# Kernel optimization log

Hardware: AMD Instinct MI355X
Metric: run time of the kernel (lower is better)

## Reference

```python
import jax, jax.numpy as jnp
import numpy as np

EPS = 1e-5

def _gather_particles(x, idx):
    # x: [B, C, M], idx: [B, N] -> [B, C, N]
    return jax.vmap(lambda a, i: a[:, i])(x, idx)

def _group_norm_dense(x, gamma, beta):
    # groups == channels (default GroupNorm(num_groups=out_channels)) -> per-channel over spatial
    m = x.mean(axis=(2, 3, 4), keepdims=True)
    v = x.var(axis=(2, 3, 4), keepdims=True)
    return (x - m) * jax.lax.rsqrt(v + EPS) * gamma[None, :, None, None, None] + beta[None, :, None, None, None]

def _group_norm_particles(x, gamma, beta):
    # x: [B, C, N]; per-channel norm over particle dim
    m = x.mean(axis=2, keepdims=True)
    v = x.var(axis=2, keepdims=True)
    return (x - m) * jax.lax.rsqrt(v + EPS) * gamma[None, :, None] + beta[None, :, None]

def _apr_conv(x, w, neighbor_idx):
    # x: [B, Cin, N]; w: [Cout, Cin, K]; neighbor_idx: [B, N, K]
    K = w.shape[2]
    out = jnp.zeros((x.shape[0], w.shape[0], x.shape[2]), x.dtype)
    for k in range(K):  # small fixed stencil
        xg = _gather_particles(x, neighbor_idx[:, :, k])  # [B, Cin, N]
        out = out + jnp.einsum('bcn,oc->bon', xg, w[:, :, k])
    return out

def setup_inputs() -> dict:
    key = jax.random.key(0)
    ks = jax.random.split(key, 12)
    B, Cin, D = 2, 64, 40
    Nc, Nf, K = 100_000, 400_000, 7
    Ch = Cin // 2  # 32
    Cout = 32
    S = D * D * D
    return {
        'x1': jax.random.normal(ks[0], (B, Cin, D, D, D), jnp.float32),
        'x2': jax.random.normal(ks[1], (B, Ch, Nf), jnp.float32),
        'w_reduce': jax.random.normal(ks[2], (Ch, Cin), jnp.float32) * 0.1,
        'gnr_gamma': jnp.ones((Ch,), jnp.float32),
        'gnr_beta': jnp.zeros((Ch,), jnp.float32),
        'w1': jax.random.normal(ks[3], (Cout, Cin, K), jnp.float32) * 0.1,
        'g1': jnp.ones((Cout,), jnp.float32),
        'b1': jnp.zeros((Cout,), jnp.float32),
        'w2': jax.random.normal(ks[4], (Cout, Cout, K), jnp.float32) * 0.1,
        'g2': jnp.ones((Cout,), jnp.float32),
        'b2': jnp.zeros((Cout,), jnp.float32),
        'sample_idx': jax.random.randint(ks[5], (B, Nc), 0, S, jnp.int32),
        'upsample_idx': jax.random.randint(ks[6], (B, Nf), 0, Nc, jnp.int32),
        'neighbor_idx': jax.random.randint(ks[7], (B, Nf, K), 0, Nf, jnp.int32),
    }

def reference(x1, x2, w_reduce, gnr_gamma, gnr_beta, w1, g1, b1, w2, g2, b2, sample_idx, upsample_idx, neighbor_idx):
    # reduce_ch: 1x1x1 conv (no bias) + GroupNorm + ReLU
    y = jnp.einsum('bcdhw,oc->bodhw', x1, w_reduce)
    y = jax.nn.relu(_group_norm_dense(y, gnr_gamma, gnr_beta))
    B, C = y.shape[0], y.shape[1]
    yf = y.reshape(B, C, -1)  # [B, C, S]
    # SampleParticles: dense voxel -> coarse particle gather
    coarse = _gather_particles(yf, sample_idx)  # [B, C, Nc]
    # UpSampleConst: coarse particle -> fine particle constant replication
    fine = _gather_particles(coarse, upsample_idx)  # [B, C, Nf]
    x = jnp.concatenate([x2, fine], axis=1)  # [B, 2C, Nf]
    # ConvBlock: two APR stencil conv + GroupNorm + ReLU blocks
    h = jax.nn.relu(_group_norm_particles(_apr_conv(x, w1, neighbor_idx), g1, b1))
    h = jax.nn.relu(_group_norm_particles(_apr_conv(h, w2, neighbor_idx), g2, b2))
    return h
```

## Files before the change

### kernel.cpp

```cpp
#include <hip/hip_runtime.h>
#include <cstdint>


typedef unsigned short u16;
typedef u16 u16x8 __attribute__((ext_vector_type(8)));
typedef float f4 __attribute__((ext_vector_type(4)));
using s16x8 = __attribute__((ext_vector_type(8))) short;
using u16x4 = __attribute__((ext_vector_type(4))) u16;

#define EPS 1e-5f
#define BB 2
#define CIN 64
#define CH 32
#define SVOX 64000
#define NC 100000
#define NF 400000

static __device__ __forceinline__ float b2f(u16 h) {
    return __builtin_bit_cast(float, (unsigned)h << 16);
}
static __device__ __forceinline__ u16 f2b(float f) {
    unsigned u = __builtin_bit_cast(unsigned, f);
    u += 0x7FFFu + ((u >> 16) & 1u);
    return (u16)(u >> 16);
}
static __device__ __forceinline__ f4 mfma16(s16x8 a, s16x8 b, f4 c) {
    return __builtin_amdgcn_mfma_f32_16x16x32_bf16(a, b, c, 0, 0, 0);
}

__global__ __launch_bounds__(256) void k_prep(
    const float* __restrict__ w1, const float* __restrict__ w2,
    float* __restrict__ stats, u16* __restrict__ wf1, u16* __restrict__ wf2)
{
    int tid = threadIdx.x;
    for (int i = tid; i < 12288; i += 256) stats[i] = 0.f;
    for (int i = tid; i < 14 * 2 * 512; i += 256) {
        int j = i & 7, l = (i >> 3) & 63, ot = (i >> 9) & 1, s = i >> 10;
        int k = s >> 1, h = s & 1;
        int c = h * 32 + (l >> 4) * 8 + j;
        int o = ot * 16 + (l & 15);
        wf1[i] = f2b(w1[(o * CIN + c) * 7 + k]);
    }
    for (int i = tid; i < 7 * 2 * 512; i += 256) {
        int j = i & 7, l = (i >> 3) & 63, ot = (i >> 9) & 1, k = i >> 10;
        int c = (l >> 4) * 8 + j;
        int o = ot * 16 + (l & 15);
        wf2[i] = f2b(w2[(o * CH + c) * 7 + k]);
    }
}

__global__ __launch_bounds__(256) void k_reduce(
    const float* __restrict__ x1, const float* __restrict__ wr,
    u16* __restrict__ y)
{
    __shared__ float wl[CIN * CH];
    int tid = threadIdx.x, b = blockIdx.y;
    for (int i = tid; i < CIN * CH; i += 256) {
        int c = i >> 5, o = i & 31;
        wl[i] = wr[o * CIN + c];
    }
    __syncthreads();
    int s0 = blockIdx.x * 512 + tid;
    int s1 = s0 + 256;
    const float* xb = x1 + (size_t)b * CIN * SVOX;
    float acc0[CH], acc1[CH];
#pragma unroll
    for (int o = 0; o < CH; o++) { acc0[o] = 0.f; acc1[o] = 0.f; }
    for (int c = 0; c < CIN; c++) {
        float xv0 = xb[(size_t)c * SVOX + s0];
        float xv1 = xb[(size_t)c * SVOX + s1];
        const float* w = &wl[c * CH];
#pragma unroll
        for (int o = 0; o < CH; o++) {
            float wv = w[o];
            acc0[o] = fmaf(xv0, wv, acc0[o]);
            acc1[o] = fmaf(xv1, wv, acc1[o]);
        }
    }
    u16* y0 = y + ((size_t)b * SVOX + s0) * CH;
    u16* y1 = y + ((size_t)b * SVOX + s1) * CH;
#pragma unroll
    for (int g = 0; g < 4; g++) {
        u16x8 v0, v1;
#pragma unroll
        for (int i = 0; i < 8; i++) {
            v0[i] = f2b(acc0[g * 8 + i]);
            v1[i] = f2b(acc1[g * 8 + i]);
        }
        ((u16x8*)y0)[g] = v0;
        ((u16x8*)y1)[g] = v1;
    }
}

__global__ __launch_bounds__(256) void k_statsB(
    const u16* __restrict__ x, float* __restrict__ stats, int rows)
{
    __shared__ float sred[CH * 2];
    int tid = threadIdx.x, b = blockIdx.y;
    if (tid < CH * 2) sred[tid] = 0.f;
    __syncthreads();
    int o = tid & 31, stripe = tid >> 5;
    const u16* xb = x + (size_t)b * rows * CH;
    int r0 = blockIdx.x * 512 + stripe * 64;
    float s = 0.f, q = 0.f;
    for (int i = 0; i < 64; i++) {
        int r = r0 + i;
        if (r < rows) {
            float v = b2f(xb[(size_t)r * CH + o]);
            s += v; q = fmaf(v, v, q);
        }
    }
    atomicAdd(&sred[o * 2], s);
    atomicAdd(&sred[o * 2 + 1], q);
    __syncthreads();
    if (tid < CH * 2) atomicAdd(&stats[(size_t)(b * CH * 2 + tid) * 32], sred[tid]);
}

__global__ void k_fin(const float* __restrict__ stats, const float* __restrict__ gamma,
                      const float* __restrict__ beta, float* __restrict__ ss, float invN)
{
    int i = threadIdx.x;
    if (i >= BB * CH) return;
    float sum = stats[(size_t)(i * 2) * 32];
    float sq  = stats[(size_t)(i * 2 + 1) * 32];
    float mean = sum * invN;
    float var = sq * invN - mean * mean;
    float rstd = rsqrtf(var + EPS);
    int o = i & 31;
    float sc = rstd * gamma[o];
    ss[i * 2] = sc;
    ss[i * 2 + 1] = beta[o] - mean * sc;
}

__global__ __launch_bounds__(256) void k_build(
    const float* __restrict__ x2, const u16* __restrict__ y,
    const float* __restrict__ ssA, const int* __restrict__ sidx,
    const int* __restrict__ uidx, u16* __restrict__ comb)
{
    __shared__ u16 tile[64][40];
    __shared__ float sl[CH * 2];
    int tid = threadIdx.x, b = blockIdx.y;
    int n0 = blockIdx.x * 64;
    if (tid < CH * 2) sl[tid] = ssA[b * CH * 2 + tid];
    int c = tid >> 3, no = (tid & 7) * 8;
    const float* src = x2 + ((size_t)b * CH + c) * NF + n0 + no;
    f4 v0 = *(const f4*)src;
    f4 v1 = *(const f4*)(src + 4);
#pragma unroll
    for (int i = 0; i < 4; i++) tile[no + i][c] = f2b(v0[i]);
#pragma unroll
    for (int i = 0; i < 4; i++) tile[no + 4 + i][c] = f2b(v1[i]);
    __syncthreads();
    int nl = tid >> 3, seg = tid & 7;
#pragma unroll
    for (int it = 0; it < 2; it++) {
        int n = n0 + it * 32 + nl;
        u16x8 ov;
        if (seg < 4) {
            int co = seg * 8;
#pragma unroll
            for (int i = 0; i < 8; i++) ov[i] = tile[it * 32 + nl][co + i];
        } else {
            int u = uidx[(size_t)b * NF + n];
            int j = sidx[(size_t)b * NC + u];
            const u16x8* yr = (const u16x8*)(y + ((size_t)b * SVOX + j) * CH);
            u16x8 v = yr[seg - 4];
            int co = (seg - 4) * 8;
#pragma unroll
            for (int i = 0; i < 8; i++)
                ov[i] = f2b(fmaxf(fmaf(b2f(v[i]), sl[(co + i) * 2], sl[(co + i) * 2 + 1]), 0.f));
        }
        *(u16x8*)(comb + ((size_t)b * NF + n) * 64 + seg * 8) = ov;
    }
}

__global__ __launch_bounds__(512) void k_conv1(
    const u16* __restrict__ comb, const u16* __restrict__ wfg,
    const int* __restrict__ nbr, u16* __restrict__ h1,
    float* __restrict__ stats1)
{
    __shared__ u16 wf[14 * 2 * 512];
    __shared__ float sst[64];
    int tid = threadIdx.x, b = blockIdx.y;
    if (tid < 64) sst[tid] = 0.f;
    const f4* wsrc = (const f4*)wfg;
    f4* wdst = (f4*)wf;
    for (int i = tid; i < 1792; i += 512) wdst[i] = wsrc[i];
    __syncthreads();
    const s16x8* wfv = (const s16x8*)wf;
    int lane = tid & 63, wave = tid >> 6;
    int p = lane & 15, q = lane >> 4;
    int n = blockIdx.x * 128 + wave * 16 + p;
    const u16* Cb = comb + (size_t)b * NF * 64;
    const int* nbb = nbr + ((size_t)b * NF + n) * 7;
    int i0[7];
#pragma unroll
    for (int k = 0; k < 7; k++) i0[k] = nbb[k];
    s16x8 rlo[7], rhi[7];
#pragma unroll
    for (int k = 0; k < 7; k++) {
        const u16* rec = Cb + (size_t)i0[k] * 64;
        rlo[k] = __builtin_bit_cast(s16x8, *(const u16x8*)(rec + q * 8));
        rhi[k] = __builtin_bit_cast(s16x8, *(const u16x8*)(rec + 32 + q * 8));
    }
    f4 acc0 = {0.f, 0.f, 0.f, 0.f};
    f4 acc1 = {0.f, 0.f, 0.f, 0.f};
#pragma unroll
    for (int k = 0; k < 7; k++) {
        acc0 = mfma16(wfv[(k * 4 + 0) * 64 + lane], rlo[k], acc0);
        acc1 = mfma16(wfv[(k * 4 + 1) * 64 + lane], rlo[k], acc1);
        acc0 = mfma16(wfv[(k * 4 + 2) * 64 + lane], rhi[k], acc0);
        acc1 = mfma16(wfv[(k * 4 + 3) * 64 + lane], rhi[k], acc1);
    }
    float s[8], t[8];
#pragma unroll
    for (int r = 0; r < 4; r++) {
        s[r] = acc0[r];     t[r] = acc0[r] * acc0[r];
        s[4 + r] = acc1[r]; t[4 + r] = acc1[r] * acc1[r];
    }
#pragma unroll
    for (int m = 1; m < 16; m <<= 1) {
#pragma unroll
        for (int j = 0; j < 8; j++) {
            s[j] += __shfl_xor(s[j], m);
            t[j] += __shfl_xor(t[j], m);
        }
    }
    if (p == 0) {
#pragma unroll
        for (int r = 0; r < 4; r++) {
            atomicAdd(&sst[(q * 4 + r) * 2],       s[r]);
            atomicAdd(&sst[(q * 4 + r) * 2 + 1],   t[r]);
            atomicAdd(&sst[(16 + q * 4 + r) * 2],     s[4 + r]);
            atomicAdd(&sst[(16 + q * 4 + r) * 2 + 1], t[4 + r]);
        }
    }
    u16x4 v0, v1;
#pragma unroll
    for (int r = 0; r < 4; r++) { v0[r] = f2b(acc0[r]); v1[r] = f2b(acc1[r]); }
    u16* out = h1 + ((size_t)b * NF + n) * CH + q * 4;
    *(u16x4*)out = v0;
    *(u16x4*)(out + 16) = v1;
    __syncthreads();
    if (tid < 64) atomicAdd(&stats1[(size_t)(b * 64 + tid) * 32], sst[tid]);
}

__global__ __launch_bounds__(512) void k_conv2(
    const u16* __restrict__ x, const u16* __restrict__ wfg,
    const int* __restrict__ nbr, const float* __restrict__ ss1,
    float* __restrict__ out, float* __restrict__ stats2)
{
    __shared__ u16 wf[7 * 2 * 512];
    __shared__ float sst[64];
    int tid = threadIdx.x, b = blockIdx.y;
    if (tid < 64) sst[tid] = 0.f;
    const f4* wsrc = (const f4*)wfg;
    f4* wdst = (f4*)wf;
    for (int i = tid; i < 896; i += 512) wdst[i] = wsrc[i];
    __syncthreads();
    const s16x8* wfv = (const s16x8*)wf;
    int lane = tid & 63, wave = tid >> 6;
    int p = lane & 15, q = lane >> 4;
    int n = blockIdx.x * 128 + wave * 16 + p;
    const u16* Xb = x + (size_t)b * NF * CH;
    const int* nbb = nbr + ((size_t)b * NF + n) * 7;
    float sc[8], sh[8];
#pragma unroll
    for (int j = 0; j < 8; j++) {
        sc[j] = ss1[(b * CH + q * 8 + j) * 2];
        sh[j] = ss1[(b * CH + q * 8 + j) * 2 + 1];
    }
    int i0[7];
#pragma unroll
    for (int k = 0; k < 7; k++) i0[k] = nbb[k];
    u16x8 raw[7];
#pragma unroll
    for (int k = 0; k < 7; k++)
        raw[k] = *(const u16x8*)(Xb + (size_t)i0[k] * CH + q * 8);
    f4 acc0 = {0.f, 0.f, 0.f, 0.f};
    f4 acc1 = {0.f, 0.f, 0.f, 0.f};
#pragma unroll
    for (int k = 0; k < 7; k++) {
        u16x8 nv;
#pragma unroll
        for (int j = 0; j < 8; j++)
            nv[j] = f2b(fmaxf(fmaf(b2f(raw[k][j]), sc[j], sh[j]), 0.f));
        s16x8 a = __builtin_bit_cast(s16x8, nv);
        acc0 = mfma16(wfv[(k * 2 + 0) * 64 + lane], a, acc0);
        acc1 = mfma16(wfv[(k * 2 + 1) * 64 + lane], a, acc1);
    }
    float s[8], t[8];
#pragma unroll
    for (int r = 0; r < 4; r++) {
        s[r] = acc0[r];     t[r] = acc0[r] * acc0[r];
        s[4 + r] = acc1[r]; t[4 + r] = acc1[r] * acc1[r];
    }
#pragma unroll
    for (int m = 1; m < 16; m <<= 1) {
#pragma unroll
        for (int j = 0; j < 8; j++) {
            s[j] += __shfl_xor(s[j], m);
            t[j] += __shfl_xor(t[j], m);
        }
    }
    if (p == 0) {
#pragma unroll
        for (int r = 0; r < 4; r++) {
            atomicAdd(&sst[(q * 4 + r) * 2],       s[r]);
            atomicAdd(&sst[(q * 4 + r) * 2 + 1],   t[r]);
            atomicAdd(&sst[(16 + q * 4 + r) * 2],     s[4 + r]);
            atomicAdd(&sst[(16 + q * 4 + r) * 2 + 1], t[4 + r]);
        }
    }
    float* ob = out + (size_t)b * CH * NF + n;
#pragma unroll
    for (int r = 0; r < 4; r++) {
        ob[(size_t)(q * 4 + r) * NF] = acc0[r];
        ob[(size_t)(16 + q * 4 + r) * NF] = acc1[r];
    }
    __syncthreads();
    if (tid < 64) atomicAdd(&stats2[(size_t)(b * 64 + tid) * 32], sst[tid]);
}

__global__ __launch_bounds__(256) void k_norm2c(
    float* __restrict__ h, const float* __restrict__ ss)
{
    int i4 = blockIdx.x * 256 + threadIdx.x;
    int cf = i4 / (NF / 4);
    float sc = ss[cf * 2], sh = ss[cf * 2 + 1];
    f4 v = ((f4*)h)[i4];
#pragma unroll
    for (int j = 0; j < 4; j++) v[j] = fmaxf(fmaf(v[j], sc, sh), 0.f);
    ((f4*)h)[i4] = v;
}

extern "C" void kernel_launch(void* const* d_in, const int* in_sizes, int n_in,
                              void* d_out, int out_size, void* d_ws, size_t ws_size,
                              hipStream_t stream)
{
    const float* x1 = (const float*)d_in[0];
    const float* x2 = (const float*)d_in[1];
    const float* wr = (const float*)d_in[2];
    const float* gA = (const float*)d_in[3];
    const float* bA = (const float*)d_in[4];
    const float* w1 = (const float*)d_in[5];
    const float* g1 = (const float*)d_in[6];
    const float* b1 = (const float*)d_in[7];
    const float* w2 = (const float*)d_in[8];
    const float* g2 = (const float*)d_in[9];
    const float* b2 = (const float*)d_in[10];
    const int* sidx = (const int*)d_in[11];
    const int* uidx = (const int*)d_in[12];
    const int* nbr  = (const int*)d_in[13];

    char* ws = (char*)d_ws;
    u16* h1      = (u16*)ws;
    u16* y       = (u16*)(ws + 51200000);
    float* stats = (float*)(ws + 59392000);
    float* statsA = stats;
    float* stats1 = (float*)(ws + 59392000 + 16384);
    float* stats2 = (float*)(ws + 59392000 + 32768);
    float* ssA    = (float*)(ws + 59392000 + 49152);
    float* ss1    = (float*)(ws + 59392000 + 49664);
    float* ss2    = (float*)(ws + 59392000 + 50176);
    u16* wf1g = (u16*)(ws + 59392000 + 50688);
    u16* wf2g = (u16*)(ws + 59392000 + 50688 + 28672);
    u16* comb = (u16*)d_out;

    k_prep<<<1, 256, 0, stream>>>(w1, w2, stats, wf1g, wf2g);
    k_reduce<<<dim3(125, BB), 256, 0, stream>>>(x1, wr, y);
    k_statsB<<<dim3(125, BB), 256, 0, stream>>>(y, statsA, SVOX);
    k_fin<<<1, 64, 0, stream>>>(statsA, gA, bA, ssA, 1.f / SVOX);
    k_build<<<dim3(6250, BB), 256, 0, stream>>>(x2, y, ssA, sidx, uidx, comb);
    k_conv1<<<dim3(3125, BB), 512, 0, stream>>>(comb, wf1g, nbr, h1, stats1);
    k_fin<<<1, 64, 0, stream>>>(stats1, g1, b1, ss1, 1.f / NF);
    k_conv2<<<dim3(3125, BB), 512, 0, stream>>>(h1, wf2g, nbr, ss1, (float*)d_out, stats2);
    k_fin<<<1, 64, 0, stream>>>(stats2, g2, b2, ss2, 1.f / NF);
    k_norm2c<<<25000, 256, 0, stream>>>((float*)d_out, ss2);
}
```

Measured before the change: 581.4 us.

## Fuse group-norm stats into reduce kernel and inline finalize into consumers

```diff
diff --git a/kernel.cpp b/kernel.cpp
--- a/kernel.cpp
+++ b/kernel.cpp
@@ -51,10 +51,12 @@
 
 __global__ __launch_bounds__(256) void k_reduce(
     const float* __restrict__ x1, const float* __restrict__ wr,
-    u16* __restrict__ y)
+    u16* __restrict__ y, float* __restrict__ statsA)
 {
     __shared__ float wl[CIN * CH];
+    __shared__ float sred[64];
     int tid = threadIdx.x, b = blockIdx.y;
+    if (tid < 64) sred[tid] = 0.f;
     for (int i = tid; i < CIN * CH; i += 256) {
         int c = i >> 5, o = i & 31;
         wl[i] = wr[o * CIN + c];
@@ -90,58 +92,55 @@
         ((u16x8*)y0)[g] = v0;
         ((u16x8*)y1)[g] = v1;
     }
-}
-
-__global__ __launch_bounds__(256) void k_statsB(
-    const u16* __restrict__ x, float* __restrict__ stats, int rows)
-{
-    __shared__ float sred[CH * 2];
-    int tid = threadIdx.x, b = blockIdx.y;
-    if (tid < CH * 2) sred[tid] = 0.f;
-    __syncthreads();
-    int o = tid & 31, stripe = tid >> 5;
-    const u16* xb = x + (size_t)b * rows * CH;
-    int r0 = blockIdx.x * 512 + stripe * 64;
-    float s = 0.f, q = 0.f;
-    for (int i = 0; i < 64; i++) {
-        int r = r0 + i;
-        if (r < rows) {
-            float v = b2f(xb[(size_t)r * CH + o]);
-            s += v; q = fmaf(v, v, q);
-        }
-    }
-    atomicAdd(&sred[o * 2], s);
-    atomicAdd(&sred[o * 2 + 1], q);
-    __syncthreads();
-    if (tid < CH * 2) atomicAdd(&stats[(size_t)(b * CH * 2 + tid) * 32], sred[tid]);
-}
-
-__global__ void k_fin(const float* __restrict__ stats, const float* __restrict__ gamma,
-                      const float* __restrict__ beta, float* __restrict__ ss, float invN)
-{
-    int i = threadIdx.x;
-    if (i >= BB * CH) return;
-    float sum = stats[(size_t)(i * 2) * 32];
-    float sq  = stats[(size_t)(i * 2 + 1) * 32];
-    float mean = sum * invN;
-    float var = sq * invN - mean * mean;
-    float rstd = rsqrtf(var + EPS);
-    int o = i & 31;
-    float sc = rstd * gamma[o];
-    ss[i * 2] = sc;
-    ss[i * 2 + 1] = beta[o] - mean * sc;
+    int lane = tid & 63;
+#pragma unroll
+    for (int g = 0; g < 4; g++) {
+        float s[8], qq[8];
+#pragma unroll
+        for (int i = 0; i < 8; i++) {
+            int o = g * 8 + i;
+            s[i] = acc0[o] + acc1[o];
+            qq[i] = fmaf(acc0[o], acc0[o], acc1[o] * acc1[o]);
+        }
+#pragma unroll
+        for (int m = 1; m < 64; m <<= 1) {
+#pragma unroll
+            for (int i = 0; i < 8; i++) {
+                s[i] += __shfl_xor(s[i], m);
+                qq[i] += __shfl_xor(qq[i], m);
+            }
+        }
+        if (lane == 0) {
+#pragma unroll
+            for (int i = 0; i < 8; i++) {
+                atomicAdd(&sred[(g * 8 + i) * 2], s[i]);
+                atomicAdd(&sred[(g * 8 + i) * 2 + 1], qq[i]);
+            }
+        }
+    }
+    __syncthreads();
+    if (tid < 64) atomicAdd(&statsA[(size_t)(b * 64 + tid) * 32], sred[tid]);
 }
 
 __global__ __launch_bounds__(256) void k_build(
     const float* __restrict__ x2, const u16* __restrict__ y,
-    const float* __restrict__ ssA, const int* __restrict__ sidx,
+    const float* __restrict__ statsA, const float* __restrict__ gA,
+    const float* __restrict__ bA, const int* __restrict__ sidx,
     const int* __restrict__ uidx, u16* __restrict__ comb)
 {
     __shared__ u16 tile[64][40];
     __shared__ float sl[CH * 2];
     int tid = threadIdx.x, b = blockIdx.y;
     int n0 = blockIdx.x * 64;
-    if (tid < CH * 2) sl[tid] = ssA[b * CH * 2 + tid];
+    if (tid < CH) {
+        float sum = statsA[(size_t)(b * 64 + tid * 2) * 32];
+        float sq  = statsA[(size_t)(b * 64 + tid * 2 + 1) * 32];
+        float mean = sum * (1.f / SVOX);
+        float var = sq * (1.f / SVOX) - mean * mean;
+        float sc = rsqrtf(var + EPS) * gA[tid];
+        sl[tid * 2] = sc;
+        sl[tid * 2 + 1] = bA[tid] - mean * sc;
+    }
     int c = tid >> 3, no = (tid & 7) * 8;
     const float* src = x2 + ((size_t)b * CH + c) * NF + n0 + no;
     f4 v0 = *(const f4*)src;
@@ -247,16 +246,27 @@
 
 __global__ __launch_bounds__(512) void k_conv2(
     const u16* __restrict__ x, const u16* __restrict__ wfg,
-    const int* __restrict__ nbr, const float* __restrict__ ss1,
+    const int* __restrict__ nbr, const float* __restrict__ stats1,
+    const float* __restrict__ g1, const float* __restrict__ b1,
     float* __restrict__ out, float* __restrict__ stats2)
 {
     __shared__ u16 wf[7 * 2 * 512];
     __shared__ float sst[64];
+    __shared__ float sl1[64];
     int tid = threadIdx.x, b = blockIdx.y;
     if (tid < 64) sst[tid] = 0.f;
     const f4* wsrc = (const f4*)wfg;
     f4* wdst = (f4*)wf;
     for (int i = tid; i < 896; i += 512) wdst[i] = wsrc[i];
+    if (tid < CH) {
+        float sum = stats1[(size_t)(b * 64 + tid * 2) * 32];
+        float sq  = stats1[(size_t)(b * 64 + tid * 2 + 1) * 32];
+        float mean = sum * (1.f / NF);
+        float var = sq * (1.f / NF) - mean * mean;
+        float sc = rsqrtf(var + EPS) * g1[tid];
+        sl1[tid * 2] = sc;
+        sl1[tid * 2 + 1] = b1[tid] - mean * sc;
+    }
     __syncthreads();
     const s16x8* wfv = (const s16x8*)wf;
     int lane = tid & 63, wave = tid >> 6;
@@ -267,8 +277,8 @@
     float sc[8], sh[8];
 #pragma unroll
     for (int j = 0; j < 8; j++) {
-        sc[j] = ss1[(b * CH + q * 8 + j) * 2];
-        sh[j] = ss1[(b * CH + q * 8 + j) * 2 + 1];
+        sc[j] = sl1[(q * 8 + j) * 2];
+        sh[j] = sl1[(q * 8 + j) * 2 + 1];
     }
     int i0[7];
 #pragma unroll
@@ -323,11 +333,18 @@
 }
 
 __global__ __launch_bounds__(256) void k_norm2c(
-    float* __restrict__ h, const float* __restrict__ ss)
+    float* __restrict__ h, const float* __restrict__ stats2,
+    const float* __restrict__ g2, const float* __restrict__ b2)
 {
     int i4 = blockIdx.x * 256 + threadIdx.x;
     int cf = i4 / (NF / 4);
-    float sc = ss[cf * 2], sh = ss[cf * 2 + 1];
+    int o = cf & 31;
+    float sum = stats2[(size_t)(cf * 2) * 32];
+    float sq  = stats2[(size_t)(cf * 2 + 1) * 32];
+    float mean = sum * (1.f / NF);
+    float var = sq * (1.f / NF) - mean * mean;
+    float sc = rsqrtf(var + EPS) * g2[o];
+    float sh = b2[o] - mean * sc;
     f4 v = ((f4*)h)[i4];
 #pragma unroll
     for (int j = 0; j < 4; j++) v[j] = fmaxf(fmaf(v[j], sc, sh), 0.f);
@@ -360,21 +377,14 @@
     float* statsA = stats;
     float* stats1 = (float*)(ws + 59392000 + 16384);
     float* stats2 = (float*)(ws + 59392000 + 32768);
-    float* ssA    = (float*)(ws + 59392000 + 49152);
-    float* ss1    = (float*)(ws + 59392000 + 49664);
-    float* ss2    = (float*)(ws + 59392000 + 50176);
-    u16* wf1g = (u16*)(ws + 59392000 + 50688);
-    u16* wf2g = (u16*)(ws + 59392000 + 50688 + 28672);
+    u16* wf1g = (u16*)(ws + 59392000 + 49152);
+    u16* wf2g = (u16*)(ws + 59392000 + 49152 + 28672);
     u16* comb = (u16*)d_out;
 
     k_prep<<<1, 256, 0, stream>>>(w1, w2, stats, wf1g, wf2g);
-    k_reduce<<<dim3(125, BB), 256, 0, stream>>>(x1, wr, y);
-    k_statsB<<<dim3(125, BB), 256, 0, stream>>>(y, statsA, SVOX);
-    k_fin<<<1, 64, 0, stream>>>(statsA, gA, bA, ssA, 1.f / SVOX);
-    k_build<<<dim3(6250, BB), 256, 0, stream>>>(x2, y, ssA, sidx, uidx, comb);
+    k_reduce<<<dim3(125, BB), 256, 0, stream>>>(x1, wr, y, statsA);
+    k_build<<<dim3(6250, BB), 256, 0, stream>>>(x2, y, statsA, gA, bA, sidx, uidx, comb);
     k_conv1<<<dim3(3125, BB), 512, 0, stream>>>(comb, wf1g, nbr, h1, stats1);
-    k_fin<<<1, 64, 0, stream>>>(stats1, g1, b1, ss1, 1.f / NF);
-    k_conv2<<<dim3(3125, BB), 512, 0, stream>>>(h1, wf2g, nbr, ss1, (float*)d_out, stats2);
-    k_fin<<<1, 64, 0, stream>>>(stats2, g2, b2, ss2, 1.f / NF);
-    k_norm2c<<<25000, 256, 0, stream>>>((float*)d_out, ss2);
-}
+    k_conv2<<<dim3(3125, BB), 512, 0, stream>>>(h1, wf2g, nbr, stats1, g1, b1, (float*)d_out, stats2);
+    k_norm2c<<<25000, 256, 0, stream>>>((float*)d_out, stats2, g2, b2);
+}
```

Measured after the change: 560.8 us. -3.5%, faster.
